# Optimization experiments

Hardware: AMD Instinct MI355X
Metric: run time of the kernel (lower is better)

## Reference

```python
import jax, jax.numpy as jnp
import numpy as np

B, S, D, H = 2, 2048, 1024, 16
HD = D // H


def setup_inputs() -> dict:
    key = jax.random.key(0)
    ks = jax.random.split(key, 9)
    std = 0.02
    return {
        "x": jax.random.normal(ks[0], (B, S, D), dtype=jnp.float32),
        "wq": jax.random.normal(ks[1], (D, D), dtype=jnp.float32) * std,
        "bq": jnp.zeros((D,), dtype=jnp.float32),
        "wk": jax.random.normal(ks[2], (D, D), dtype=jnp.float32) * std,
        "bk": jnp.zeros((D,), dtype=jnp.float32),
        "wv": jax.random.normal(ks[3], (D, D), dtype=jnp.float32) * std,
        "bv": jnp.zeros((D,), dtype=jnp.float32),
        "wo": jax.random.normal(ks[4], (D, D), dtype=jnp.float32) * std,
        "bo": jnp.zeros((D,), dtype=jnp.float32),
    }


def reference(x, wq, bq, wk, bk, wv, bv, wo, bo):
    bsz, seq_len, d_model = x.shape
    # projections: torch Linear computes x @ W.T + b with W of shape (out, in)
    q = (x @ wq.T + bq).reshape(bsz, seq_len, H, HD).transpose(0, 2, 1, 3)  # bhsd
    k = (x @ wk.T + bk).reshape(bsz, seq_len, H, HD).transpose(0, 2, 1, 3)
    v = (x @ wv.T + bv).reshape(bsz, seq_len, H, HD).transpose(0, 2, 1, 3)
    scale = HD ** -0.5
    scores = jnp.einsum("bhqd,bhkd->bhqk", q, k) * scale  # [B,H,S,S]
    causal = jnp.tril(jnp.ones((seq_len, seq_len), dtype=bool))
    scores = jnp.where(causal[None, None], scores, -jnp.inf)
    attn = jax.nn.softmax(scores, axis=-1)
    ctx = jnp.einsum("bhqk,bhkd->bhqd", attn, v)
    ctx = ctx.transpose(0, 2, 1, 3).reshape(bsz, seq_len, d_model)
    return ctx @ wo.T + bo
```

## Files before the change

### kernel.cpp

```cpp
#include <hip/hip_runtime.h>
#include <hip/hip_bf16.h>

#define B_  2
#define S_  2048
#define D_  1024
#define H_  16
#define HD_ 64
#define M_  (B_ * S_)

typedef __bf16 bf16;
typedef __bf16 bf16x4 __attribute__((ext_vector_type(4)));
typedef __bf16 bf16x8 __attribute__((ext_vector_type(8)));
typedef float  f32x4  __attribute__((ext_vector_type(4)));
typedef float  f32x16 __attribute__((ext_vector_type(16)));
typedef unsigned int uint;

__device__ __forceinline__ bf16x8 ld8g(const bf16* p) { return *(const bf16x8*)p; }

#define GLL(g, l) __builtin_amdgcn_global_load_lds( \
    (const __attribute__((address_space(1))) void*)(g), \
    (__attribute__((address_space(3))) void*)(l), 16, 0, 0)

#define SWZ(row, byteoff) (((row) * 128) + ((byteoff) ^ (((row) & 7) << 4)))

__global__ __launch_bounds__(256) void convert_kernel(
    const float* __restrict__ x,  const float* __restrict__ wq,
    const float* __restrict__ wk, const float* __restrict__ wv,
    const float* __restrict__ wo,
    bf16* __restrict__ xb,  bf16* __restrict__ wqb, bf16* __restrict__ wkb,
    bf16* __restrict__ wvb, bf16* __restrict__ wob)
{
    const int seg = blockIdx.y;
    const float* src;
    bf16* dst;
    if (seg < 4)      { src = x  + (long)seg * 1048576; dst = xb  + (long)seg * 1048576; }
    else if (seg == 4){ src = wq; dst = wqb; }
    else if (seg == 5){ src = wk; dst = wkb; }
    else if (seg == 6){ src = wv; dst = wvb; }
    else              { src = wo; dst = wob; }
    const long i = ((long)blockIdx.x * 256 + threadIdx.x) * 8;
    float4 a = *(const float4*)(src + i);
    float4 b = *(const float4*)(src + i + 4);
    bf16x8 r;
    r[0] = (bf16)a.x; r[1] = (bf16)a.y; r[2] = (bf16)a.z; r[3] = (bf16)a.w;
    r[4] = (bf16)b.x; r[5] = (bf16)b.y; r[6] = (bf16)b.z; r[7] = (bf16)b.w;
    *(bf16x8*)(dst + i) = r;
}

__device__ __forceinline__ void gemm_acc_bk32(
    const bf16* __restrict__ A, const bf16* __restrict__ Bt,
    f32x4 (&acc)[4][4])
{
    __shared__ bf16 As[128 * 32];
    __shared__ bf16 Bs[128 * 32];

    const int tid  = threadIdx.x;
    const int wave = tid >> 6;
    const int lane = tid & 63;
    const int quad = lane >> 4;
    const int l15  = lane & 15;
    const int wr   = (wave >> 1) * 64;
    const int wc   = (wave & 1) * 64;
    const int m0   = blockIdx.y * 128;
    const int n0   = blockIdx.x * 128;

    const int sr = wave * 16 + (lane >> 2);
    const int sc = (lane & 3) * 8;
    const bf16* Ag = A  + (long)(m0 + sr) * D_ + sc;
    const bf16* Bg = Bt + (long)(n0 + sr) * D_ + sc;
    bf16* lA = As + wave * 512;
    bf16* lB = Bs + wave * 512;

    for (int k0 = 0; k0 < D_; k0 += 32) {
        __syncthreads();
        GLL(Ag + k0,             lA);
        GLL(Ag + 64 * D_ + k0,   lA + 64 * 32);
        GLL(Bg + k0,             lB);
        GLL(Bg + 64 * D_ + k0,   lB + 64 * 32);
        __syncthreads();

        bf16x8 af[4], bfr[4];
        for (int mi = 0; mi < 4; mi++)
            af[mi] = *(const bf16x8*)&As[(wr + mi * 16 + l15) * 32 + quad * 8];
        for (int ni = 0; ni < 4; ni++)
            bfr[ni] = *(const bf16x8*)&Bs[(wc + ni * 16 + l15) * 32 + quad * 8];

        for (int mi = 0; mi < 4; mi++)
            for (int ni = 0; ni < 4; ni++)
                acc[mi][ni] = __builtin_amdgcn_mfma_f32_16x16x32_bf16(
                    af[mi], bfr[ni], acc[mi][ni], 0, 0, 0);
    }
}

__global__ __launch_bounds__(256) void gemm_qkv(
    const bf16* __restrict__ xb,
    const bf16* __restrict__ wqb, const bf16* __restrict__ wkb, const bf16* __restrict__ wvb,
    const float* __restrict__ bq, const float* __restrict__ bk, const float* __restrict__ bv,
    bf16* __restrict__ qb, bf16* __restrict__ kb, bf16* __restrict__ vt)
{
    const bf16*  Bt   = (blockIdx.z == 0) ? wqb : (blockIdx.z == 1) ? wkb : wvb;
    const float* bias = (blockIdx.z == 0) ? bq  : (blockIdx.z == 1) ? bk  : bv;

    f32x4 acc[4][4] = {};
    gemm_acc_bk32(xb, Bt, acc);

    const int lane = threadIdx.x & 63;
    const int wave = threadIdx.x >> 6;
    const int quad = lane >> 4;
    const int l15  = lane & 15;
    const int wr   = (wave >> 1) * 64;
    const int wc   = (wave & 1) * 64;
    const int m0   = blockIdx.y * 128;
    const int n0   = blockIdx.x * 128;

    if (blockIdx.z < 2) {
        bf16* Cout = (blockIdx.z == 0) ? qb : kb;
        for (int ni = 0; ni < 4; ni++) {
            const int col = n0 + wc + ni * 16 + l15;
            const float bv = bias[col];
            for (int mi = 0; mi < 4; mi++) {
                const int rowb = m0 + wr + mi * 16 + quad * 4;
                for (int r = 0; r < 4; r++)
                    Cout[(long)(rowb + r) * D_ + col] = (bf16)(acc[mi][ni][r] + bv);
            }
        }
    } else {
        for (int ni = 0; ni < 4; ni++) {
            const int col = n0 + wc + ni * 16 + l15;
            const float bv = bias[col];
            const int h = col >> 6, hd = col & (HD_ - 1);
            for (int mi = 0; mi < 4; mi++) {
                const int rowb = m0 + wr + mi * 16 + quad * 4;
                const int b = rowb >> 11;
                const int s0 = rowb & (S_ - 1);
                bf16x4 v4;
                for (int r = 0; r < 4; r++) v4[r] = (bf16)(acc[mi][ni][r] + bv);
                *(bf16x4*)&vt[(((long)(b * H_ + h)) * HD_ + hd) * S_ + s0] = v4;
            }
        }
    }
}

__global__ __launch_bounds__(256) void gemm_out(
    const bf16* __restrict__ cb, const bf16* __restrict__ wob,
    const float* __restrict__ bo, float* __restrict__ out)
{
    __shared__ bf16 As[64 * 32];
    __shared__ bf16 Bs[128 * 32];

    const int tid  = threadIdx.x;
    const int wave = tid >> 6;
    const int lane = tid & 63;
    const int quad = lane >> 4;
    const int l15  = lane & 15;
    const int wr   = (wave >> 1) * 32;
    const int wc   = (wave & 1) * 64;
    const int m0   = blockIdx.y * 64;
    const int n0   = blockIdx.x * 128;

    const int sr = tid >> 2;
    const int scg = (tid & 3) * 8;
    const bf16* Ag = cb  + (long)(m0 + sr) * D_ + scg;
    const bf16* Bg = wob + (long)(n0 + sr) * D_ + scg;
    bf16* lA = As + wave * 512;
    bf16* lB = Bs + wave * 512;

    f32x4 acc[2][4] = {};
    for (int k0 = 0; k0 < D_; k0 += 32) {
        __syncthreads();
        GLL(Ag + k0,            lA);
        GLL(Bg + k0,            lB);
        GLL(Bg + 64 * D_ + k0,  lB + 64 * 32);
        __syncthreads();

        bf16x8 af[2], bfr[4];
        for (int mi = 0; mi < 2; mi++)
            af[mi] = *(const bf16x8*)&As[(wr + mi * 16 + l15) * 32 + quad * 8];
        for (int ni = 0; ni < 4; ni++)
            bfr[ni] = *(const bf16x8*)&Bs[(wc + ni * 16 + l15) * 32 + quad * 8];

        for (int mi = 0; mi < 2; mi++)
            for (int ni = 0; ni < 4; ni++)
                acc[mi][ni] = __builtin_amdgcn_mfma_f32_16x16x32_bf16(
                    af[mi], bfr[ni], acc[mi][ni], 0, 0, 0);
    }

    for (int ni = 0; ni < 4; ni++) {
        const int col = n0 + wc + ni * 16 + l15;
        const float bv = bo[col];
        for (int mi = 0; mi < 2; mi++) {
            const int rowb = m0 + wr + mi * 16 + quad * 4;
            for (int r = 0; r < 4; r++)
                out[(long)(rowb + r) * D_ + col] = acc[mi][ni][r] + bv;
        }
    }
}

__global__ __launch_bounds__(256) void attn_kernel(
    const bf16* __restrict__ Q, const bf16* __restrict__ K,
    const bf16* __restrict__ vt, bf16* __restrict__ ctx)
{
    __shared__ bf16 Ks[2][64 * 64];
    __shared__ bf16 Vt[2][64 * 64];

    const int tid  = threadIdx.x;
    const int wave = tid >> 6;
    const int lane = tid & 63;
    const int l31  = lane & 31;
    const int hi   = lane >> 5;
    const int hi16 = hi * 16;
    const int hi4  = hi * 4;
    const int bh   = blockIdx.y;
    const int qt   = (blockIdx.y < 16) ? blockIdx.x : (15 - (int)blockIdx.x);
    const int b    = bh >> 4, h = bh & 15;
    const long base = ((long)b * S_) * D_ + h * HD_;
    const bf16* Kg  = K + base;
    const bf16* Vth = vt + (long)bh * HD_ * S_;

    char* K0 = (char*)&Ks[0][0]; char* K1 = (char*)&Ks[1][0];
    char* V0 = (char*)&Vt[0][0]; char* V1 = (char*)&Vt[1][0];

    const int r0 = tid >> 3;
    const int c0 = (tid & 7) * 8;
    const int cB = (tid & 7) * 16;

    const int qw   = qt * 128 + wave * 32;
    const int qrow = qw + l31;
    const bf16* Qr = Q + base + (long)qrow * D_;
    bf16x8 qf0 = ld8g(Qr + 0  + hi * 8);
    bf16x8 qf1 = ld8g(Qr + 16 + hi * 8);
    bf16x8 qf2 = ld8g(Qr + 32 + hi * 8);
    bf16x8 qf3 = ld8g(Qr + 48 + hi * 8);

    float l_i = 0.f;
    f32x16 oA = {}, oB = {};

    auto process_tile = [&](int kbase, int buf) {
        if (kbase > qw + 31) return;
        const char* Kb = buf ? K1 : K0;
        const char* Vb = buf ? V1 : V0;
        #pragma unroll
        for (int s = 0; s < 2; s++) {
            const int kb = kbase + 32 * s;
            if (kb > qw + 31) continue;
            f32x16 sa = {};
            __builtin_amdgcn_s_setprio(1);
            {
                bf16x8 a0 = *(const bf16x8*)(Kb + SWZ(32 * s + l31, 0   + hi16));
                bf16x8 a1 = *(const bf16x8*)(Kb + SWZ(32 * s + l31, 32  + hi16));
                bf16x8 a2 = *(const bf16x8*)(Kb + SWZ(32 * s + l31, 64  + hi16));
                bf16x8 a3 = *(const bf16x8*)(Kb + SWZ(32 * s + l31, 96  + hi16));
                sa = __builtin_amdgcn_mfma_f32_32x32x16_bf16(a0, qf0, sa, 0, 0, 0);
                sa = __builtin_amdgcn_mfma_f32_32x32x16_bf16(a1, qf1, sa, 0, 0, 0);
                sa = __builtin_amdgcn_mfma_f32_32x32x16_bf16(a2, qf2, sa, 0, 0, 0);
                sa = __builtin_amdgcn_mfma_f32_32x32x16_bf16(a3, qf3, sa, 0, 0, 0);
            }
            __builtin_amdgcn_s_setprio(0);

            float p[16];
            float loc = 0.f;
            if (kb + 31 <= qw) {
                #pragma unroll
                for (int r = 0; r < 16; r++) { p[r] = __expf(sa[r] * 0.125f); loc += p[r]; }
            } else {
                #pragma unroll
                for (int r = 0; r < 16; r++) {
                    const int kg = kb + (r & 3) + 8 * (r >> 2) + hi4;
                    p[r] = (kg <= qrow) ? __expf(sa[r] * 0.125f) : 0.f;
                    loc += p[r];
                }
            }
            l_i += loc + __shfl_xor(loc, 32, 64);

            uint w[8], sw[8];
            #pragma unroll
            for (int t = 0; t < 8; t++) {
                union { uint u; bf16 h2[2]; } pk;
                pk.h2[0] = (bf16)p[2 * t];
                pk.h2[1] = (bf16)p[2 * t + 1];
                w[t] = pk.u;
            }
            #pragma unroll
            for (int t = 0; t < 8; t++)
                sw[t] = (uint)__shfl_xor((int)w[t], 32, 64);

            __builtin_amdgcn_s_setprio(1);
            #pragma unroll
            for (int cc = 0; cc < 2; cc++) {
                union { uint u[4]; bf16x8 v; } pa;
                pa.u[0] = hi ? sw[4 * cc + 2] : w[4 * cc];
                pa.u[1] = hi ? sw[4 * cc + 3] : w[4 * cc + 1];
                pa.u[2] = hi ? w[4 * cc + 2]  : sw[4 * cc];
                pa.u[3] = hi ? w[4 * cc + 3]  : sw[4 * cc + 1];
                const int kc = 2 * s + cc;
                bf16x8 vb0 = *(const bf16x8*)(Vb + SWZ(l31,      kc * 32 + hi16));
                bf16x8 vb1 = *(const bf16x8*)(Vb + SWZ(32 + l31, kc * 32 + hi16));
                oA = __builtin_amdgcn_mfma_f32_32x32x16_bf16(pa.v, vb0, oA, 0, 0, 0);
                oB = __builtin_amdgcn_mfma_f32_32x32x16_bf16(pa.v, vb1, oB, 0, 0, 0);
            }
            __builtin_amdgcn_s_setprio(0);
        }
    };

    bf16x8 kA0 = ld8g(Kg + (long)r0 * D_ + c0);
    bf16x8 kA1 = ld8g(Kg + (long)(r0 + 32) * D_ + c0);
    bf16x8 wA0 = ld8g(Vth + (long)r0 * S_ + c0);
    bf16x8 wA1 = ld8g(Vth + (long)(r0 + 32) * S_ + c0);
    bf16x8 kB0 = ld8g(Kg + (long)(64 + r0) * D_ + c0);
    bf16x8 kB1 = ld8g(Kg + (long)(64 + r0 + 32) * D_ + c0);
    bf16x8 wB0 = ld8g(Vth + (long)r0 * S_ + 64 + c0);
    bf16x8 wB1 = ld8g(Vth + (long)(r0 + 32) * S_ + 64 + c0);

    const int njt = 2 * qt + 2;
    for (int j = 0; j < njt; j += 2) {
        __syncthreads();
        *(bf16x8*)(K0 + SWZ(r0,      cB)) = kA0;
        *(bf16x8*)(K0 + SWZ(r0 + 32, cB)) = kA1;
        *(bf16x8*)(V0 + SWZ(r0,      cB)) = wA0;
        *(bf16x8*)(V0 + SWZ(r0 + 32, cB)) = wA1;
        *(bf16x8*)(K1 + SWZ(r0,      cB)) = kB0;
        *(bf16x8*)(K1 + SWZ(r0 + 32, cB)) = kB1;
        *(bf16x8*)(V1 + SWZ(r0,      cB)) = wB0;
        *(bf16x8*)(V1 + SWZ(r0 + 32, cB)) = wB1;
        if (j + 2 < njt) {
            kA0 = ld8g(Kg + (long)((j + 2) * 64 + r0) * D_ + c0);
            kA1 = ld8g(Kg + (long)((j + 2) * 64 + r0 + 32) * D_ + c0);
            wA0 = ld8g(Vth + (long)r0 * S_ + (j + 2) * 64 + c0);
            wA1 = ld8g(Vth + (long)(r0 + 32) * S_ + (j + 2) * 64 + c0);
            kB0 = ld8g(Kg + (long)((j + 3) * 64 + r0) * D_ + c0);
            kB1 = ld8g(Kg + (long)((j + 3) * 64 + r0 + 32) * D_ + c0);
            wB0 = ld8g(Vth + (long)r0 * S_ + (j + 3) * 64 + c0);
            wB1 = ld8g(Vth + (long)(r0 + 32) * S_ + (j + 3) * 64 + c0);
        }
        __syncthreads();
        process_tile(j * 64, 0);
        process_tile(j * 64 + 64, 1);
    }

    __syncthreads();
    char* epi = (char*)&Ks[0][0] + wave * 4096;
    const float inv = 1.f / l_i;
    #pragma unroll
    for (int r = 0; r < 16; r++) {
        const int qr = (r & 3) + 8 * (r >> 2) + hi4;
        const float si = __shfl(inv, qr, 64);
        *(bf16*)(epi + SWZ(qr, l31 * 2))      = (bf16)(oA[r] * si);
        *(bf16*)(epi + SWZ(qr, 64 + l31 * 2)) = (bf16)(oB[r] * si);
    }
    __asm__ volatile("s_waitcnt lgkmcnt(0)" ::: "memory");
    #pragma unroll
    for (int round = 0; round < 4; round++) {
        const int rowq = (lane >> 3) + round * 8;
        bf16x8 val = *(const bf16x8*)(epi + SWZ(rowq, (lane & 7) * 16));
        const int q_g = qt * 128 + wave * 32 + rowq;
        *(bf16x8*)&ctx[base + (long)q_g * D_ + (lane & 7) * 8] = val;
    }
}

extern "C" void kernel_launch(void* const* d_in, const int* in_sizes, int n_in,
                              void* d_out, int out_size, void* d_ws, size_t ws_size,
                              hipStream_t stream)
{
    const float* x  = (const float*)d_in[0];
    const float* wq = (const float*)d_in[1];
    const float* bq = (const float*)d_in[2];
    const float* wk = (const float*)d_in[3];
    const float* bk = (const float*)d_in[4];
    const float* wv = (const float*)d_in[5];
    const float* bv = (const float*)d_in[6];
    const float* wo = (const float*)d_in[7];
    const float* bo = (const float*)d_in[8];
    float* out = (float*)d_out;

    const long NX = (long)M_ * D_;
    const long NW = (long)D_ * D_;
    bf16* xb  = (bf16*)d_ws;
    bf16* wqb = xb  + NX;
    bf16* wkb = wqb + NW;
    bf16* wvb = wkb + NW;
    bf16* wob = wvb + NW;
    bf16* qb  = wob + NW;
    bf16* kb  = qb  + NX;
    bf16* vt  = kb  + NX;
    bf16* cb  = xb;

    dim3 blk(256, 1, 1);

    convert_kernel<<<dim3(512, 8), blk, 0, stream>>>(
        x, wq, wk, wv, wo, xb, wqb, wkb, wvb, wob);

    gemm_qkv<<<dim3(8, 32, 3), blk, 0, stream>>>(
        xb, wqb, wkb, wvb, bq, bk, bv, qb, kb, vt);

    attn_kernel<<<dim3(16, 32), blk, 0, stream>>>(qb, kb, vt, cb);

    gemm_out<<<dim3(8, 64), blk, 0, stream>>>(cb, wob, bo, out);
}
```

Baseline: 191.2 us.

## Split attention block into 8 waves of 16 query rows using 16x16 MFMA

```diff
diff --git a/kernel.cpp b/kernel.cpp
--- a/kernel.cpp
+++ b/kernel.cpp
@@ -12,7 +12,6 @@
 typedef __bf16 bf16x4 __attribute__((ext_vector_type(4)));
 typedef __bf16 bf16x8 __attribute__((ext_vector_type(8)));
 typedef float  f32x4  __attribute__((ext_vector_type(4)));
-typedef float  f32x16 __attribute__((ext_vector_type(16)));
 typedef unsigned int uint;
 
 __device__ __forceinline__ bf16x8 ld8g(const bf16* p) { return *(const bf16x8*)p; }
@@ -196,7 +195,7 @@
     }
 }
 
-__global__ __launch_bounds__(256) void attn_kernel(
+__global__ __launch_bounds__(512, 4) void attn_kernel(
     const bf16* __restrict__ Q, const bf16* __restrict__ K,
     const bf16* __restrict__ vt, bf16* __restrict__ ctx)
 {
@@ -206,10 +205,8 @@
     const int tid  = threadIdx.x;
     const int wave = tid >> 6;
     const int lane = tid & 63;
-    const int l31  = lane & 31;
-    const int hi   = lane >> 5;
-    const int hi16 = hi * 16;
-    const int hi4  = hi * 4;
+    const int quad = lane >> 4;
+    const int l15  = lane & 15;
     const int bh   = blockIdx.y;
     const int qt   = (blockIdx.y < 16) ? blockIdx.x : (15 - (int)blockIdx.x);
     const int b    = bh >> 4, h = bh & 15;
@@ -223,114 +220,97 @@
     const int r0 = tid >> 3;
     const int c0 = (tid & 7) * 8;
     const int cB = (tid & 7) * 16;
-
-    const int qw   = qt * 128 + wave * 32;
-    const int qrow = qw + l31;
+    const int pr = (r0 & 32) + ((r0 >> 2) & 1) * 16 + ((r0 >> 3) & 3) * 4 + (r0 & 3);
+
+    const int qw   = qt * 128 + wave * 16;
+    const int qrow = qw + l15;
     const bf16* Qr = Q + base + (long)qrow * D_;
-    bf16x8 qf0 = ld8g(Qr + 0  + hi * 8);
-    bf16x8 qf1 = ld8g(Qr + 16 + hi * 8);
-    bf16x8 qf2 = ld8g(Qr + 32 + hi * 8);
-    bf16x8 qf3 = ld8g(Qr + 48 + hi * 8);
+    bf16x8 qf0 = ld8g(&Qr[quad * 8]);
+    bf16x8 qf1 = ld8g(&Qr[quad * 8 + 32]);
 
     float l_i = 0.f;
-    f32x16 oA = {}, oB = {};
+    f32x4 o_acc[4] = {};
 
     auto process_tile = [&](int kbase, int buf) {
-        if (kbase > qw + 31) return;
+        if (kbase > qw + 15) return;
         const char* Kb = buf ? K1 : K0;
         const char* Vb = buf ? V1 : V0;
+
+        f32x4 sc[4];
+        __builtin_amdgcn_s_setprio(1);
         #pragma unroll
-        for (int s = 0; s < 2; s++) {
-            const int kb = kbase + 32 * s;
-            if (kb > qw + 31) continue;
-            f32x16 sa = {};
-            __builtin_amdgcn_s_setprio(1);
-            {
-                bf16x8 a0 = *(const bf16x8*)(Kb + SWZ(32 * s + l31, 0   + hi16));
-                bf16x8 a1 = *(const bf16x8*)(Kb + SWZ(32 * s + l31, 32  + hi16));
-                bf16x8 a2 = *(const bf16x8*)(Kb + SWZ(32 * s + l31, 64  + hi16));
-                bf16x8 a3 = *(const bf16x8*)(Kb + SWZ(32 * s + l31, 96  + hi16));
-                sa = __builtin_amdgcn_mfma_f32_32x32x16_bf16(a0, qf0, sa, 0, 0, 0);
-                sa = __builtin_amdgcn_mfma_f32_32x32x16_bf16(a1, qf1, sa, 0, 0, 0);
-                sa = __builtin_amdgcn_mfma_f32_32x32x16_bf16(a2, qf2, sa, 0, 0, 0);
-                sa = __builtin_amdgcn_mfma_f32_32x32x16_bf16(a3, qf3, sa, 0, 0, 0);
-            }
-            __builtin_amdgcn_s_setprio(0);
-
-            float p[16];
-            float loc = 0.f;
-            if (kb + 31 <= qw) {
+        for (int kt = 0; kt < 4; kt++) {
+            bf16x8 a0 = *(const bf16x8*)(Kb + SWZ(kt * 16 + l15, quad * 16));
+            bf16x8 a1 = *(const bf16x8*)(Kb + SWZ(kt * 16 + l15, quad * 16 + 64));
+            f32x4 z = {};
+            z = __builtin_amdgcn_mfma_f32_16x16x32_bf16(a0, qf0, z, 0, 0, 0);
+            z = __builtin_amdgcn_mfma_f32_16x16x32_bf16(a1, qf1, z, 0, 0, 0);
+            sc[kt] = z;
+        }
+        __builtin_amdgcn_s_setprio(0);
+
+        float sum = 0.f;
+        if (kbase + 63 <= qw) {
+            #pragma unroll
+            for (int kt = 0; kt < 4; kt++)
                 #pragma unroll
-                for (int r = 0; r < 16; r++) { p[r] = __expf(sa[r] * 0.125f); loc += p[r]; }
-            } else {
+                for (int r = 0; r < 4; r++) {
+                    const float p = __expf(sc[kt][r] * 0.125f);
+                    sc[kt][r] = p;
+                    sum += p;
+                }
+        } else {
+            #pragma unroll
+            for (int kt = 0; kt < 4; kt++)
                 #pragma unroll
-                for (int r = 0; r < 16; r++) {
-                    const int kg = kb + (r & 3) + 8 * (r >> 2) + hi4;
-                    p[r] = (kg <= qrow) ? __expf(sa[r] * 0.125f) : 0.f;
-                    loc += p[r];
+                for (int r = 0; r < 4; r++) {
+                    const int kg = kbase + (kt >> 1) * 32 + quad * 8 + (kt & 1) * 4 + r;
+                    const float p = (kg <= qrow) ? __expf(sc[kt][r] * 0.125f) : 0.f;
+                    sc[kt][r] = p;
+                    sum += p;
                 }
-            }
-            l_i += loc + __shfl_xor(loc, 32, 64);
-
-            uint w[8], sw[8];
-            #pragma unroll
-            for (int t = 0; t < 8; t++) {
-                union { uint u; bf16 h2[2]; } pk;
-                pk.h2[0] = (bf16)p[2 * t];
-                pk.h2[1] = (bf16)p[2 * t + 1];
-                w[t] = pk.u;
-            }
-            #pragma unroll
-            for (int t = 0; t < 8; t++)
-                sw[t] = (uint)__shfl_xor((int)w[t], 32, 64);
-
-            __builtin_amdgcn_s_setprio(1);
-            #pragma unroll
-            for (int cc = 0; cc < 2; cc++) {
-                union { uint u[4]; bf16x8 v; } pa;
-                pa.u[0] = hi ? sw[4 * cc + 2] : w[4 * cc];
-                pa.u[1] = hi ? sw[4 * cc + 3] : w[4 * cc + 1];
-                pa.u[2] = hi ? w[4 * cc + 2]  : sw[4 * cc];
-                pa.u[3] = hi ? w[4 * cc + 3]  : sw[4 * cc + 1];
-                const int kc = 2 * s + cc;
-                bf16x8 vb0 = *(const bf16x8*)(Vb + SWZ(l31,      kc * 32 + hi16));
-                bf16x8 vb1 = *(const bf16x8*)(Vb + SWZ(32 + l31, kc * 32 + hi16));
-                oA = __builtin_amdgcn_mfma_f32_32x32x16_bf16(pa.v, vb0, oA, 0, 0, 0);
-                oB = __builtin_amdgcn_mfma_f32_32x32x16_bf16(pa.v, vb1, oB, 0, 0, 0);
-            }
-            __builtin_amdgcn_s_setprio(0);
-        }
+        }
+        sum += __shfl_xor(sum, 16, 64);
+        sum += __shfl_xor(sum, 32, 64);
+        l_i += sum;
+
+        union { bf16 hh[8]; bf16x8 v; } pa0, pa1;
+        #pragma unroll
+        for (int r = 0; r < 4; r++) {
+            pa0.hh[r]     = (bf16)sc[0][r];
+            pa0.hh[r + 4] = (bf16)sc[1][r];
+            pa1.hh[r]     = (bf16)sc[2][r];
+            pa1.hh[r + 4] = (bf16)sc[3][r];
+        }
+
+        __builtin_amdgcn_s_setprio(1);
+        #pragma unroll
+        for (int ni = 0; ni < 4; ni++) {
+            bf16x8 av0 = *(const bf16x8*)(Vb + SWZ(ni * 16 + l15, quad * 16));
+            bf16x8 av1 = *(const bf16x8*)(Vb + SWZ(ni * 16 + l15, quad * 16 + 64));
+            o_acc[ni] = __builtin_amdgcn_mfma_f32_16x16x32_bf16(av0, pa0.v, o_acc[ni], 0, 0, 0);
+            o_acc[ni] = __builtin_amdgcn_mfma_f32_16x16x32_bf16(av1, pa1.v, o_acc[ni], 0, 0, 0);
+        }
+        __builtin_amdgcn_s_setprio(0);
     };
 
-    bf16x8 kA0 = ld8g(Kg + (long)r0 * D_ + c0);
-    bf16x8 kA1 = ld8g(Kg + (long)(r0 + 32) * D_ + c0);
-    bf16x8 wA0 = ld8g(Vth + (long)r0 * S_ + c0);
-    bf16x8 wA1 = ld8g(Vth + (long)(r0 + 32) * S_ + c0);
-    bf16x8 kB0 = ld8g(Kg + (long)(64 + r0) * D_ + c0);
-    bf16x8 kB1 = ld8g(Kg + (long)(64 + r0 + 32) * D_ + c0);
-    bf16x8 wB0 = ld8g(Vth + (long)r0 * S_ + 64 + c0);
-    bf16x8 wB1 = ld8g(Vth + (long)(r0 + 32) * S_ + 64 + c0);
+    bf16x8 kA = ld8g(Kg + (long)r0 * D_ + c0);
+    bf16x8 wA = ld8g(Vth + (long)r0 * S_ + c0);
+    bf16x8 kB = ld8g(Kg + (long)(64 + r0) * D_ + c0);
+    bf16x8 wB = ld8g(Vth + (long)r0 * S_ + 64 + c0);
 
     const int njt = 2 * qt + 2;
     for (int j = 0; j < njt; j += 2) {
         __syncthreads();
-        *(bf16x8*)(K0 + SWZ(r0,      cB)) = kA0;
-        *(bf16x8*)(K0 + SWZ(r0 + 32, cB)) = kA1;
-        *(bf16x8*)(V0 + SWZ(r0,      cB)) = wA0;
-        *(bf16x8*)(V0 + SWZ(r0 + 32, cB)) = wA1;
-        *(bf16x8*)(K1 + SWZ(r0,      cB)) = kB0;
-        *(bf16x8*)(K1 + SWZ(r0 + 32, cB)) = kB1;
-        *(bf16x8*)(V1 + SWZ(r0,      cB)) = wB0;
-        *(bf16x8*)(V1 + SWZ(r0 + 32, cB)) = wB1;
+        *(bf16x8*)(K0 + SWZ(pr, cB)) = kA;
+        *(bf16x8*)(V0 + SWZ(r0, cB)) = wA;
+        *(bf16x8*)(K1 + SWZ(pr, cB)) = kB;
+        *(bf16x8*)(V1 + SWZ(r0, cB)) = wB;
         if (j + 2 < njt) {
-            kA0 = ld8g(Kg + (long)((j + 2) * 64 + r0) * D_ + c0);
-            kA1 = ld8g(Kg + (long)((j + 2) * 64 + r0 + 32) * D_ + c0);
-            wA0 = ld8g(Vth + (long)r0 * S_ + (j + 2) * 64 + c0);
-            wA1 = ld8g(Vth + (long)(r0 + 32) * S_ + (j + 2) * 64 + c0);
-            kB0 = ld8g(Kg + (long)((j + 3) * 64 + r0) * D_ + c0);
-            kB1 = ld8g(Kg + (long)((j + 3) * 64 + r0 + 32) * D_ + c0);
-            wB0 = ld8g(Vth + (long)r0 * S_ + (j + 3) * 64 + c0);
-            wB1 = ld8g(Vth + (long)(r0 + 32) * S_ + (j + 3) * 64 + c0);
+            kA = ld8g(Kg + (long)((j + 2) * 64 + r0) * D_ + c0);
+            wA = ld8g(Vth + (long)r0 * S_ + (j + 2) * 64 + c0);
+            kB = ld8g(Kg + (long)((j + 3) * 64 + r0) * D_ + c0);
+            wB = ld8g(Vth + (long)r0 * S_ + (j + 3) * 64 + c0);
         }
         __syncthreads();
         process_tile(j * 64, 0);
@@ -338,21 +318,24 @@
     }
 
     __syncthreads();
-    char* epi = (char*)&Ks[0][0] + wave * 4096;
+    char* epi = (char*)&Ks[0][0] + wave * 2048;
     const float inv = 1.f / l_i;
     #pragma unroll
-    for (int r = 0; r < 16; r++) {
-        const int qr = (r & 3) + 8 * (r >> 2) + hi4;
-        const float si = __shfl(inv, qr, 64);
-        *(bf16*)(epi + SWZ(qr, l31 * 2))      = (bf16)(oA[r] * si);
-        *(bf16*)(epi + SWZ(qr, 64 + l31 * 2)) = (bf16)(oB[r] * si);
+    for (int ni = 0; ni < 4; ni++) {
+        union { uint2 u; bf16 hh[4]; } pk;
+        pk.hh[0] = (bf16)(o_acc[ni][0] * inv);
+        pk.hh[1] = (bf16)(o_acc[ni][1] * inv);
+        pk.hh[2] = (bf16)(o_acc[ni][2] * inv);
+        pk.hh[3] = (bf16)(o_acc[ni][3] * inv);
+        *(uint2*)(epi + SWZ(l15, ni * 32 + quad * 8)) = pk.u;
     }
     __asm__ volatile("s_waitcnt lgkmcnt(0)" ::: "memory");
+    __builtin_amdgcn_sched_barrier(0);
     #pragma unroll
-    for (int round = 0; round < 4; round++) {
+    for (int round = 0; round < 2; round++) {
         const int rowq = (lane >> 3) + round * 8;
         bf16x8 val = *(const bf16x8*)(epi + SWZ(rowq, (lane & 7) * 16));
-        const int q_g = qt * 128 + wave * 32 + rowq;
+        const int q_g = qt * 128 + wave * 16 + rowq;
         *(bf16x8*)&ctx[base + (long)q_g * D_ + (lane & 7) * 8] = val;
     }
 }
@@ -392,7 +375,7 @@
     gemm_qkv<<<dim3(8, 32, 3), blk, 0, stream>>>(
         xb, wqb, wkb, wvb, bq, bk, bv, qb, kb, vt);
 
-    attn_kernel<<<dim3(16, 32), blk, 0, stream>>>(qb, kb, vt, cb);
+    attn_kernel<<<dim3(16, 32), dim3(512, 1, 1), 0, stream>>>(qb, kb, vt, cb);
 
     gemm_out<<<dim3(8, 64), blk, 0, stream>>>(cb, wob, bo, out);
 }
```

After: 177.6 us. 1.08x faster.
